# Kernel optimization log

Measured on AMD Instinct MI355X. Metric: run time of the kernel, lower is better.

Reference implementation:

```python
import jax, jax.numpy as jnp
import numpy as np

def setup_inputs() -> dict:
    key = jax.random.key(0)
    k1, k2, k3, k4 = jax.random.split(key, 4)
    B, S, IN, OUT = 4, 2048, 4096, 11008
    x = jax.random.normal(k1, (B, S, IN), dtype=jnp.float32)
    int8_weight = jax.random.randint(k2, (OUT, IN), -128, 128, dtype=jnp.int32)
    scale = jax.random.uniform(k3, (1,), dtype=jnp.float32) * 0.01 + 1e-4
    bias = jax.random.normal(k4, (OUT,), dtype=jnp.float32)
    return {"x": x, "int8_weight": int8_weight, "scale": scale, "bias": bias}

def reference(x, int8_weight, scale, bias):
    # dequantize int8 weight with per-tensor scale, then linear: y = x @ W^T + b
    weight = int8_weight.astype(jnp.float32) * scale[0]  # [OUT, IN]
    return jnp.einsum('bsi,oi->bso', x, weight) + bias
```

## Files before the change

### kernel.cpp

```cpp
#include <hip/hip_runtime.h>
#include <stdint.h>

typedef __attribute__((ext_vector_type(4))) int   int4v;
typedef __attribute__((ext_vector_type(4))) float f32x4;

#define K_DIM 4096
#define N_DIM 11008
#define M_DIM 8192
#define BM 256
#define BN 256
#define BKB 128
#define NT (K_DIM / BKB)
#define MT2 (M_DIM / BM)
#define NT2 (N_DIM / BN)

__global__ __launch_bounds__(256) void quant_x_kernel(
    const float* __restrict__ x, unsigned char* __restrict__ xq,
    float* __restrict__ srow)
{
    const int row = blockIdx.x;
    const float4* xr = (const float4*)(x + (size_t)row * K_DIM);
    float4 v[4];
    float m = 0.f;
    #pragma unroll
    for (int i = 0; i < 4; ++i) {
        v[i] = xr[threadIdx.x + 256 * i];
        m = fmaxf(m, fmaxf(fmaxf(fabsf(v[i].x), fabsf(v[i].y)),
                           fmaxf(fabsf(v[i].z), fabsf(v[i].w))));
    }
    #pragma unroll
    for (int off = 32; off; off >>= 1) m = fmaxf(m, __shfl_xor(m, off, 64));
    __shared__ float wmax[4];
    if ((threadIdx.x & 63) == 0) wmax[threadIdx.x >> 6] = m;
    __syncthreads();
    const float mb  = fmaxf(fmaxf(wmax[0], wmax[1]), fmaxf(wmax[2], wmax[3]));
    const float s   = (mb > 0.f) ? mb * (1.f / 127.f) : 1.f;
    const float inv = (mb > 0.f) ? 127.f / mb : 0.f;
    if (threadIdx.x == 0) srow[row] = s;
    uint32_t* oq = (uint32_t*)(xq + (size_t)row * K_DIM);
    #pragma unroll
    for (int i = 0; i < 4; ++i) {
        int a = __float2int_rn(v[i].x * inv), b = __float2int_rn(v[i].y * inv);
        int c = __float2int_rn(v[i].z * inv), d = __float2int_rn(v[i].w * inv);
        oq[threadIdx.x + 256 * i] =
            (a & 0xff) | ((b & 0xff) << 8) | ((c & 0xff) << 16) | ((d & 0xff) << 24);
    }
}

__global__ void cvt_w8_kernel(const int* __restrict__ w,
                              uint2* __restrict__ wq, int n8) {
    int i = blockIdx.x * blockDim.x + threadIdx.x;
    if (i >= n8) return;
    const int4* p = (const int4*)w + 2 * (size_t)i;
    int4 a = p[0], b = p[1];
    uint32_t lo = (a.x & 0xff) | ((a.y & 0xff) << 8) | ((a.z & 0xff) << 16) | ((a.w & 0xff) << 24);
    uint32_t hi = (b.x & 0xff) | ((b.y & 0xff) << 8) | ((b.z & 0xff) << 16) | ((b.w & 0xff) << 24);
    wq[i] = (uint2){lo, hi};
}

#define GLDS16(gsrc, ldst)                                                       \
    __builtin_amdgcn_global_load_lds(                                            \
        (const __attribute__((address_space(1))) void*)(gsrc),                   \
        (__attribute__((address_space(3))) void*)(ldst), 16, 0, 0)

#define SCHED0()  __builtin_amdgcn_sched_barrier(0)
#define BARRIER() __builtin_amdgcn_s_barrier()
#define VMCNT(n)  asm volatile("s_waitcnt vmcnt(" #n ")" ::: "memory")
#define LGKM0()   do { asm volatile("s_waitcnt lgkmcnt(0)" ::: "memory"); SCHED0(); } while (0)
#define LGKM8()   do { asm volatile("s_waitcnt lgkmcnt(8)" ::: "memory"); SCHED0(); } while (0)

__global__ __launch_bounds__(512, 2) void gemm2_kernel(
    const unsigned char* __restrict__ xq,
    const unsigned char* __restrict__ wq,
    const float* __restrict__ srow,
    const float* __restrict__ scale,
    const float* __restrict__ bias,
    float* __restrict__ out)
{
    __shared__ unsigned char sm[131072];
    char* smc = (char*)sm;

    const int T  = threadIdx.x;
    const int l  = T & 63;
    const int wv = T >> 6;
    const int wm = wv >> 2;
    const int wn = wv & 3;

    const int orig = blockIdx.x;
    const int xcd  = orig & 7;
    const int p    = orig >> 3;
    const int bm   = xcd * 4 + (p & 3);
    const int bn   = p >> 2;
    const size_t rowM0 = (size_t)bm * BM;
    const size_t rowN0 = (size_t)bn * BN;

    const int rowT = T >> 3;
    const int colT = (((T & 7) * 16) ^ ((rowT & 7) << 4));
    const unsigned char* pAg = xq + (rowM0 + rowT) * (size_t)K_DIM + colT;
    const unsigned char* pBg = wq + (rowN0 + ((rowT >> 5) << 6) + (rowT & 31)) * (size_t)K_DIM + colT;

    auto stageA = [&](char* base, int Q, int kt) {
        #pragma unroll
        for (int c = 0; c < 2; ++c) {
            const unsigned char* src = pAg + (size_t)(c * 128 + Q * 64) * K_DIM + (size_t)kt * BKB;
            char* dst = base + Q * 16384 + c * 8192 + T * 16;
            GLDS16(src, dst);
        }
    };
    auto stageB = [&](char* base, int Q, int kt) {
        #pragma unroll
        for (int c = 0; c < 2; ++c) {
            const unsigned char* src = pBg + (size_t)(c * 128 + Q * 32) * K_DIM + (size_t)kt * BKB;
            char* dst = base + 32768 + Q * 16384 + c * 8192 + T * 16;
            GLDS16(src, dst);
        }
    };

    const int sw     = (l & 7) << 4;
    const int inrow0 = (l >> 4) * 16;
    const int lowk0  = inrow0 ^ sw;
    const int lowk1  = (64 + inrow0) ^ sw;
    const int arow   = wm * 64 + (l & 15);
    const int brow   = wn * 32 + (l & 15);

    int4v acc[8][4];
    #pragma unroll
    for (int i = 0; i < 8; ++i)
        #pragma unroll
        for (int j = 0; j < 4; ++j)
            acc[i][j] = (int4v){0, 0, 0, 0};

    int4v Ah[4][2];
    int4v Bh[4][2];

    char* const b0 = smc;
    char* const b1 = smc + 65536;

#define READ_A(base)                                                             \
    _Pragma("unroll")                                                            \
    for (int im = 0; im < 4; ++im) {                                             \
        Ah[im][0] = *(const int4v*)((base) + (arow + im * 16) * 128 + lowk0);    \
        Ah[im][1] = *(const int4v*)((base) + (arow + im * 16) * 128 + lowk1);    \
    }
#define READ_B(base, f0)                                                         \
    _Pragma("unroll")                                                            \
    for (int f = 0; f < 2; ++f) {                                                \
        Bh[(f0) + f][0] = *(const int4v*)((base) + (brow + f * 16) * 128 + lowk0); \
        Bh[(f0) + f][1] = *(const int4v*)((base) + (brow + f * 16) * 128 + lowk1); \
    }
#define MFMAQ(mi, ni)                                                            \
    __builtin_amdgcn_s_setprio(1);                                               \
    _Pragma("unroll")                                                            \
    for (int im = 0; im < 4; ++im)                                               \
        _Pragma("unroll")                                                        \
        for (int jn = 0; jn < 2; ++jn)                                           \
            _Pragma("unroll")                                                    \
            for (int kk = 0; kk < 2; ++kk)                                       \
                acc[(mi) + im][(ni) + jn] = __builtin_amdgcn_mfma_i32_16x16x64_i8( \
                    Ah[im][kk], Bh[(ni) + jn][kk], acc[(mi) + im][(ni) + jn], 0, 0, 0); \
    __builtin_amdgcn_s_setprio(0);

#define TILE_BODY(bcur, EE, STN)                                                 \
                                                                         \
    READ_A(bcur);                                                                \
    READ_B((bcur) + 32768, 0);                                                   \
    LGKM8();                                                                     \
    BARRIER(); SCHED0();                                                         \
    LGKM0();                                                                     \
    MFMAQ(0, 0);                                                                 \
    BARRIER(); SCHED0();                                                         \
                                                                         \
    READ_B((bcur) + 32768 + 16384, 2);                                           \
    if (STN) stageA((bcur), 0, (EE) + 2);                                        \
    BARRIER(); SCHED0();                                                         \
    LGKM0();                                                                     \
    MFMAQ(0, 2);                                                                 \
    BARRIER(); SCHED0();                                                         \
                                                                         \
    READ_A((bcur) + 16384);                                                      \
    if (STN) stageB((bcur), 0, (EE) + 2);                                        \
    BARRIER(); SCHED0();                                                         \
    LGKM0();                                                                     \
    MFMAQ(4, 0);                                                                 \
    BARRIER(); SCHED0();                                                         \
                                                                         \
    if (STN) { stageB((bcur), 1, (EE) + 2); stageA((bcur), 1, (EE) + 2); }       \
    BARRIER(); SCHED0();                                                         \
    MFMAQ(4, 2);                                                                 \
    if (STN) VMCNT(8); else VMCNT(0);                                            \
    BARRIER(); SCHED0();

    stageA(b0, 0, 0); stageB(b0, 0, 0); stageB(b0, 1, 0); stageA(b0, 1, 0);
    stageA(b1, 0, 1); stageB(b1, 0, 1); stageB(b1, 1, 1); stageA(b1, 1, 1);
    VMCNT(8);
    BARRIER(); SCHED0();

    for (int kt2 = 0; kt2 < NT / 2; ++kt2) {
        const int  E   = kt2 * 2;
        const bool st0 = (E + 2 < NT);
        const bool st1 = (E + 3 < NT);
        TILE_BODY(b0, E,     st0);
        TILE_BODY(b1, E + 1, st1);
    }

    const float s = scale[0];
    #pragma unroll
    for (int fm = 0; fm < 8; ++fm) {
        const size_t row0 = rowM0 + wm * 128 + fm * 16 + (l >> 4) * 4;
        const float4 sr4 = *(const float4*)(srow + row0);
        #pragma unroll
        for (int fn = 0; fn < 4; ++fn) {
            const int col = (int)rowN0 + wn * 64 + fn * 16 + (l & 15);
            const float bv = bias[col];
            float* o = out + row0 * N_DIM + col;
            o[0]                  = (float)acc[fm][fn][0] * (sr4.x * s) + bv;
            o[(size_t)1 * N_DIM]  = (float)acc[fm][fn][1] * (sr4.y * s) + bv;
            o[(size_t)2 * N_DIM]  = (float)acc[fm][fn][2] * (sr4.z * s) + bv;
            o[(size_t)3 * N_DIM]  = (float)acc[fm][fn][3] * (sr4.w * s) + bv;
        }
    }
}

extern "C" void kernel_launch(void* const* d_in, const int* in_sizes, int n_in,
                              void* d_out, int out_size, void* d_ws, size_t ws_size,
                              hipStream_t stream) {
    const float* x     = (const float*)d_in[0];
    const int*   w     = (const int*)d_in[1];
    const float* scale = (const float*)d_in[2];
    const float* bias  = (const float*)d_in[3];
    float*       out   = (float*)d_out;

    const size_t x_elems = (size_t)M_DIM * K_DIM;
    const size_t w_elems = (size_t)N_DIM * K_DIM;
    const size_t xq_off  = 0;
    const size_t wq_off  = x_elems;
    const size_t sr_off  = x_elems + w_elems;
    if (ws_size < sr_off + (size_t)M_DIM * 4) return;

    unsigned char* xqp = (unsigned char*)d_ws + xq_off;
    unsigned char* wqp = (unsigned char*)d_ws + wq_off;
    float*         srp = (float*)((unsigned char*)d_ws + sr_off);

    quant_x_kernel<<<M_DIM, 256, 0, stream>>>(x, xqp, srp);
    {
        int n8 = (int)(w_elems / 8);
        cvt_w8_kernel<<<(n8 + 255) / 256, 256, 0, stream>>>(w, (uint2*)wqp, n8);
    }
    gemm2_kernel<<<MT2 * NT2, 512, 0, stream>>>(xqp, wqp, srp, scale, bias, out);
}
```

Before: 452.6 us.

## Restructure GEMM k-tile schedule into two half-phases with deferred A staging

Cuts each k-tile body from four MFMA quarter-phases to two half-phases, each doing 32 MFMAs with all four B fragments loaded up front. The explicit lgkmcnt waits and several barriers go away, which reduces synchronisation per tile. The second A-half staging of the next buffer is moved into the following tile body, and the vmcnt accounting is adjusted to match. This costs more live B registers, and with fewer explicit LDS waits the compiler has to insert them itself. It also raises correctness risk in the staging and wait bookkeeping.

```diff
diff --git a/kernel.cpp b/kernel.cpp
--- a/kernel.cpp
+++ b/kernel.cpp
@@ -66,8 +66,6 @@
 #define SCHED0()  __builtin_amdgcn_sched_barrier(0)
 #define BARRIER() __builtin_amdgcn_s_barrier()
 #define VMCNT(n)  asm volatile("s_waitcnt vmcnt(" #n ")" ::: "memory")
-#define LGKM0()   do { asm volatile("s_waitcnt lgkmcnt(0)" ::: "memory"); SCHED0(); } while (0)
-#define LGKM8()   do { asm volatile("s_waitcnt lgkmcnt(8)" ::: "memory"); SCHED0(); } while (0)
 
 __global__ __launch_bounds__(512, 2) void gemm2_kernel(
     const unsigned char* __restrict__ xq,
@@ -148,59 +146,50 @@
         Bh[(f0) + f][0] = *(const int4v*)((base) + (brow + f * 16) * 128 + lowk0); \
         Bh[(f0) + f][1] = *(const int4v*)((base) + (brow + f * 16) * 128 + lowk1); \
     }
-#define MFMAQ(mi, ni)                                                            \
+#define MFMAH(mi)                                                                \
     __builtin_amdgcn_s_setprio(1);                                               \
     _Pragma("unroll")                                                            \
     for (int im = 0; im < 4; ++im)                                               \
         _Pragma("unroll")                                                        \
-        for (int jn = 0; jn < 2; ++jn)                                           \
+        for (int jn = 0; jn < 4; ++jn)                                           \
             _Pragma("unroll")                                                    \
             for (int kk = 0; kk < 2; ++kk)                                       \
-                acc[(mi) + im][(ni) + jn] = __builtin_amdgcn_mfma_i32_16x16x64_i8( \
-                    Ah[im][kk], Bh[(ni) + jn][kk], acc[(mi) + im][(ni) + jn], 0, 0, 0); \
+                acc[(mi) + im][jn] = __builtin_amdgcn_mfma_i32_16x16x64_i8(      \
+                    Ah[im][kk], Bh[jn][kk], acc[(mi) + im][jn], 0, 0, 0);        \
     __builtin_amdgcn_s_setprio(0);
 
-#define TILE_BODY(bcur, EE, STN)                                                 \
-                                                                         \
+#define TILE_BODY(bcur, bnxt, EE, STA1, STPA)                                    \
+    \
     READ_A(bcur);                                                                \
     READ_B((bcur) + 32768, 0);                                                   \
-    LGKM8();                                                                     \
+    READ_B((bcur) + 49152, 2);                                                   \
+    if (STA1) stageA((bnxt), 1, (EE) + 1);                                       \
+    if (STA1) VMCNT(8); else VMCNT(0);                                           \
     BARRIER(); SCHED0();                                                         \
-    LGKM0();                                                                     \
-    MFMAQ(0, 0);                                                                 \
+    MFMAH(0);                                                                    \
+    SCHED0();                                                                    \
+       \
+    READ_A((bcur) + 16384);                                                      \
+    if (STPA) { stageA((bcur), 0, (EE) + 2); stageB((bcur), 0, (EE) + 2);        \
+                stageB((bcur), 1, (EE) + 2); }                                   \
     BARRIER(); SCHED0();                                                         \
-                                                                         \
-    READ_B((bcur) + 32768 + 16384, 2);                                           \
-    if (STN) stageA((bcur), 0, (EE) + 2);                                        \
-    BARRIER(); SCHED0();                                                         \
-    LGKM0();                                                                     \
-    MFMAQ(0, 2);                                                                 \
-    BARRIER(); SCHED0();                                                         \
-                                                                         \
-    READ_A((bcur) + 16384);                                                      \
-    if (STN) stageB((bcur), 0, (EE) + 2);                                        \
-    BARRIER(); SCHED0();                                                         \
-    LGKM0();                                                                     \
-    MFMAQ(4, 0);                                                                 \
-    BARRIER(); SCHED0();                                                         \
-                                                                         \
-    if (STN) { stageB((bcur), 1, (EE) + 2); stageA((bcur), 1, (EE) + 2); }       \
-    BARRIER(); SCHED0();                                                         \
-    MFMAQ(4, 2);                                                                 \
-    if (STN) VMCNT(8); else VMCNT(0);                                            \
+    MFMAH(4);                                                                    \
+    if (STPA) VMCNT(8); else { if (STA1) VMCNT(2); else VMCNT(0); }              \
     BARRIER(); SCHED0();
 
-    stageA(b0, 0, 0); stageB(b0, 0, 0); stageB(b0, 1, 0); stageA(b0, 1, 0);
-    stageA(b1, 0, 1); stageB(b1, 0, 1); stageB(b1, 1, 1); stageA(b1, 1, 1);
+    stageA(b0, 0, 0); stageB(b0, 0, 0); stageB(b0, 1, 0);
+    stageA(b0, 1, 0);
+    stageA(b1, 0, 1); stageB(b1, 0, 1); stageB(b1, 1, 1);
     VMCNT(8);
     BARRIER(); SCHED0();
 
     for (int kt2 = 0; kt2 < NT / 2; ++kt2) {
         const int  E   = kt2 * 2;
-        const bool st0 = (E + 2 < NT);
-        const bool st1 = (E + 3 < NT);
-        TILE_BODY(b0, E,     st0);
-        TILE_BODY(b1, E + 1, st1);
+        const bool stp = (E + 2 < NT);
+        TILE_BODY(b0, b1, E, true, stp);
+        const bool sa1 = (E + 2 < NT);
+        const bool sp1 = (E + 3 < NT);
+        TILE_BODY(b1, b0, E + 1, sa1, sp1);
     }
 
     const float s = scale[0];
```

Measured after the change: 443.8 us. About the same (-1.9%).
